# Performance work log

Hardware: AMD Instinct MI355X
Metric: run time of the kernel (lower is better)

The kernel has to match this reference:

```python
import jax, jax.numpy as jnp
import numpy as np

EMBED_DIM = 1024
NUM_HEADS = 16
HEAD_DIM = EMBED_DIM // NUM_HEADS
B, NQ, K = 2, 2048, 2048


def setup_inputs() -> dict:
    key = jax.random.key(0)
    ks = jax.random.split(key, 11)
    s = 1.0 / np.sqrt(EMBED_DIM)
    return {
        "Q_input": jax.random.normal(ks[0], (B, NQ, EMBED_DIM), jnp.float32),
        "K_input": jax.random.normal(ks[1], (B, K, EMBED_DIM), jnp.float32),
        "V_input": jax.random.normal(ks[2], (B, K, EMBED_DIM), jnp.float32),
        "Wq": jax.random.normal(ks[3], (EMBED_DIM, EMBED_DIM), jnp.float32) * s,
        "bq": jnp.zeros((EMBED_DIM,), jnp.float32),
        "Wk": jax.random.normal(ks[4], (EMBED_DIM, EMBED_DIM), jnp.float32) * s,
        "bk": jnp.zeros((EMBED_DIM,), jnp.float32),
        "Wv": jax.random.normal(ks[5], (EMBED_DIM, EMBED_DIM), jnp.float32) * s,
        "bv": jnp.zeros((EMBED_DIM,), jnp.float32),
        "Wo": jax.random.normal(ks[6], (EMBED_DIM, EMBED_DIM), jnp.float32) * s,
        "bo": jnp.zeros((EMBED_DIM,), jnp.float32),
    }


def reference(Q_input, K_input, V_input, Wq, bq, Wk, bk, Wv, bv, Wo, bo):
    b, n_q, _ = Q_input.shape
    k = K_input.shape[1]
    # Linear projections (torch Linear: x @ W.T + b)
    Q = Q_input @ Wq.T + bq
    Kp = K_input @ Wk.T + bk
    V = V_input @ Wv.T + bv
    # [b, h, s, d]
    Q = Q.reshape(b, n_q, NUM_HEADS, HEAD_DIM).transpose(0, 2, 1, 3)
    Kp = Kp.reshape(b, k, NUM_HEADS, HEAD_DIM).transpose(0, 2, 1, 3)
    V = V.reshape(b, k, NUM_HEADS, HEAD_DIM).transpose(0, 2, 1, 3)
    scores = jnp.einsum("bhqd,bhkd->bhqk", Q, Kp) / jnp.sqrt(jnp.float32(HEAD_DIM))
    weights = jax.nn.softmax(scores, axis=-1)
    attn = jnp.einsum("bhqk,bhkd->bhqd", weights, V)
    attn = attn.transpose(0, 2, 1, 3).reshape(b, n_q, EMBED_DIM)
    return attn @ Wo.T + bo
```

## Files before the change

kernel.cpp:

```cpp
#include <hip/hip_runtime.h>
#include <hip/hip_bf16.h>

typedef __bf16  bf16x8 __attribute__((ext_vector_type(8)));
typedef float   f32x4  __attribute__((ext_vector_type(4)));
typedef float   f32x16 __attribute__((ext_vector_type(16)));

#define EMB   1024
#define QSTR  3072
#define HD    64
#define NH    16
#define SEQ   2048
#define BATCH 2
#define TOKENS (BATCH*SEQ)
#define TK    64

typedef __attribute__((address_space(1))) unsigned int* gp_t;
typedef __attribute__((address_space(3))) unsigned int* lp_t;
__device__ __forceinline__ void gload16(const __bf16* g, __bf16* l) {
    __builtin_amdgcn_global_load_lds((gp_t)(unsigned long long)(const void*)g,
                                     (lp_t)(unsigned int)(unsigned long long)(void*)l,
                                     16, 0, 0);
}

__device__ __forceinline__ unsigned int pack2(float a, float b) {
    unsigned short u0 = __builtin_bit_cast(unsigned short, (__bf16)a);
    unsigned short u1 = __builtin_bit_cast(unsigned short, (__bf16)b);
    return (unsigned int)u0 | ((unsigned int)u1 << 16);
}

__global__ __launch_bounds__(256) void cvt4_kernel(
    const float* __restrict__ s0, const float* __restrict__ s1,
    const float* __restrict__ s2, const float* __restrict__ s3,
    __bf16* __restrict__ dst, int n_per)
{
    const float* s = (blockIdx.y == 0) ? s0 : (blockIdx.y == 1) ? s1
                   : (blockIdx.y == 2) ? s2 : s3;
    int i = (blockIdx.x * 256 + threadIdx.x) * 8;
    if (i >= n_per) return;
    float4 a = *(const float4*)(s + i);
    float4 b = *(const float4*)(s + i + 4);
    __bf16 o[8] = {(__bf16)a.x, (__bf16)a.y, (__bf16)a.z, (__bf16)a.w,
                   (__bf16)b.x, (__bf16)b.y, (__bf16)b.z, (__bf16)b.w};
    *(uint4*)(dst + (size_t)blockIdx.y * n_per + i) = *(const uint4*)o;
}

__global__ __launch_bounds__(256, 3) void gemm_qkv(
    const __bf16* __restrict__ X, const __bf16* __restrict__ Wt,
    const float* __restrict__ b0, const float* __restrict__ b1,
    const float* __restrict__ b2, __bf16* __restrict__ Y)
{
    __shared__ __align__(16) __bf16 As[2][128 * 32];
    __shared__ __align__(16) __bf16 Bs[2][128 * 32];

    const int tid  = threadIdx.x;
    const int wave = tid >> 6;
    const int lane = tid & 63;
    const int quad = lane >> 4;
    const int l16  = lane & 15;
    const int warp_m = wave >> 1;
    const int warp_n = wave & 1;

    const int bm = blockIdx.y;
    const int bn = blockIdx.x;

    const int lr = lane >> 2;
    const int lc = (lane & 3) ^ ((lr >> 1) & 3);
    const __bf16* Ag = X + (size_t)(bn >> 3) * TOKENS * EMB
                         + (size_t)(bm * 128 + wave * 32 + lr) * EMB + lc * 8;
    const __bf16* Bg = Wt + (size_t)(bn * 128 + wave * 32 + lr) * EMB + lc * 8;
    const int off = wave * 1024;

    f32x4 acc[4][4] = {};

    gload16(Ag,            As[0] + off);
    gload16(Ag + 16 * EMB, As[0] + off + 512);
    gload16(Bg,            Bs[0] + off);
    gload16(Bg + 16 * EMB, Bs[0] + off + 512);

    for (int t = 0; t < EMB / 32; ++t) {
        const int cur = t & 1, nxt = cur ^ 1;
        __syncthreads();
        if (t + 1 < EMB / 32) {
            const __bf16* a0 = Ag + (t + 1) * 32;
            const __bf16* w0 = Bg + (t + 1) * 32;
            gload16(a0,            As[nxt] + off);
            gload16(a0 + 16 * EMB, As[nxt] + off + 512);
            gload16(w0,            Bs[nxt] + off);
            gload16(w0 + 16 * EMB, Bs[nxt] + off + 512);
        }

        bf16x8 af[4], bf[4];
        #pragma unroll
        for (int i = 0; i < 4; ++i) {
            int rowa = warp_m * 64 + i * 16 + l16;
            int rowb = warp_n * 64 + i * 16 + l16;
            af[i] = *(const bf16x8*)(As[cur] + (rowa * 4 + (quad ^ ((rowa >> 1) & 3))) * 8);
            bf[i] = *(const bf16x8*)(Bs[cur] + (rowb * 4 + (quad ^ ((rowb >> 1) & 3))) * 8);
        }
        #pragma unroll
        for (int i = 0; i < 4; ++i)
            #pragma unroll
            for (int j = 0; j < 4; ++j)
                acc[i][j] = __builtin_amdgcn_mfma_f32_16x16x32_bf16(af[i], bf[j], acc[i][j], 0, 0, 0);
    }

    #pragma unroll
    for (int i = 0; i < 4; ++i)
        #pragma unroll
        for (int j = 0; j < 4; ++j) {
            int n = bn * 128 + warp_n * 64 + j * 16 + l16;
            const float* bsel = (n < 1024) ? b0 : (n < 2048) ? b1 : b2;
            float bj = bsel[n & 1023];
            #pragma unroll
            for (int r = 0; r < 4; ++r) {
                int m = bm * 128 + warp_m * 64 + i * 16 + quad * 4 + r;
                Y[(size_t)m * QSTR + n] = (__bf16)(acc[i][j][r] + bj);
            }
        }
}

template <typename TY>
__global__ __launch_bounds__(256) void gemm_fast(
    const __bf16* __restrict__ X, const __bf16* __restrict__ Wt,
    const float* __restrict__ b0, TY* __restrict__ Y, int ldy)
{
    __shared__ __align__(16) __bf16 As[2][128 * 64];
    __shared__ __align__(16) __bf16 Bs[2][64 * 64];

    const int tid  = threadIdx.x;
    const int wave = tid >> 6;
    const int lane = tid & 63;
    const int quad = lane >> 4;
    const int l16  = lane & 15;
    const int warp_m = wave >> 1;
    const int warp_n = wave & 1;

    const int bm = blockIdx.y;
    const int bn = blockIdx.x;

    const int lr = lane >> 3;
    const int lc = (lane & 7) ^ lr;
    const __bf16* Ag = X + (size_t)(bm * 128 + wave * 32 + lr) * EMB + lc * 8;
    const __bf16* Bg = Wt + (size_t)(bn * 64 + wave * 16 + lr) * EMB + lc * 8;
    const int aoff = wave * 2048;
    const int boff = wave * 1024;

    f32x4 acc[4][2] = {};

    gload16(Ag,            As[0] + aoff);
    gload16(Ag +  8 * EMB, As[0] + aoff + 512);
    gload16(Ag + 16 * EMB, As[0] + aoff + 1024);
    gload16(Ag + 24 * EMB, As[0] + aoff + 1536);
    gload16(Bg,            Bs[0] + boff);
    gload16(Bg +  8 * EMB, Bs[0] + boff + 512);

    for (int t = 0; t < EMB / 64; ++t) {
        const int cur = t & 1, nxt = cur ^ 1;
        __syncthreads();
        if (t + 1 < EMB / 64) {
            const __bf16* a0 = Ag + (t + 1) * 64;
            const __bf16* w0 = Bg + (t + 1) * 64;
            gload16(a0,            As[nxt] + aoff);
            gload16(a0 +  8 * EMB, As[nxt] + aoff + 512);
            gload16(a0 + 16 * EMB, As[nxt] + aoff + 1024);
            gload16(a0 + 24 * EMB, As[nxt] + aoff + 1536);
            gload16(w0,            Bs[nxt] + boff);
            gload16(w0 +  8 * EMB, Bs[nxt] + boff + 512);
        }

        #pragma unroll
        for (int kk = 0; kk < 2; ++kk) {
            bf16x8 af[4], bf[2];
            #pragma unroll
            for (int i = 0; i < 4; ++i) {
                int row = warp_m * 64 + i * 16 + l16;
                af[i] = *(const bf16x8*)(As[cur] + (row * 8 + ((kk * 4 + quad) ^ (row & 7))) * 8);
            }
            #pragma unroll
            for (int j = 0; j < 2; ++j) {
                int row = warp_n * 32 + j * 16 + l16;
                bf[j] = *(const bf16x8*)(Bs[cur] + (row * 8 + ((kk * 4 + quad) ^ (row & 7))) * 8);
            }
            #pragma unroll
            for (int i = 0; i < 4; ++i)
                #pragma unroll
                for (int j = 0; j < 2; ++j)
                    acc[i][j] = __builtin_amdgcn_mfma_f32_16x16x32_bf16(af[i], bf[j], acc[i][j], 0, 0, 0);
        }
    }

    #pragma unroll
    for (int i = 0; i < 4; ++i)
        #pragma unroll
        for (int j = 0; j < 2; ++j) {
            int n = bn * 64 + warp_n * 32 + j * 16 + l16;
            float bj = b0[n];
            #pragma unroll
            for (int r = 0; r < 4; ++r) {
                int m = bm * 128 + warp_m * 64 + i * 16 + quad * 4 + r;
                Y[(size_t)m * ldy + n] = (TY)(acc[i][j][r] + bj);
            }
        }
}

__global__ __launch_bounds__(256) void attn_kernel(
    const __bf16* __restrict__ QKV, __bf16* __restrict__ Op)
{
    __shared__ __align__(16) __bf16 Ks[2][64][64];
    __shared__ __align__(16) __bf16 Vt[2][64][72];

    const int tid  = threadIdx.x;
    const int wave = tid >> 6;
    const int lane = tid & 63;
    const int l31  = lane & 31;
    const int hi   = lane >> 5;
    const int e7   = l31 & 7;

    const int qt = blockIdx.x;
    const int h  = blockIdx.y;
    const int b  = blockIdx.z;

    const size_t qoff  = (size_t)b * SEQ * QSTR + (size_t)h * HD;
    const size_t obase = (size_t)b * SEQ * EMB  + (size_t)h * HD;
    const int qbase = qt * 128 + wave * 32;

    bf16x8 aq[4];
    {
        const __bf16* qrow = QKV + qoff + (size_t)(qbase + l31) * QSTR + hi * 8;
        #pragma unroll
        for (int dc = 0; dc < 4; ++dc) {
            bf16x8 v = *(const bf16x8*)(qrow + dc * 16);
            #pragma unroll
            for (int i = 0; i < 8; ++i) v[i] = (__bf16)((float)v[i] * 0.125f);
            aq[dc] = v;
        }
    }

    float  l_run   = 0.f;
    f32x16 oacc[2] = {};

    const __bf16* Kg = QKV + qoff + EMB;
    const __bf16* Vg = QKV + qoff + 2 * EMB;

    const int srow = tid >> 3;
    const int scol = (tid & 7) << 3;
    const int sch  = tid & 7;
    const int kp0  = (sch ^ (srow & 7)) << 3;
    const int g0 = srow >> 3;
    const int g1 = g0 + 4;

    {
        uint4 k0 = *(const uint4*)(Kg + (size_t)(srow     ) * QSTR + scol);
        uint4 k1 = *(const uint4*)(Kg + (size_t)(srow + 32) * QSTR + scol);
        uint4 v0 = *(const uint4*)(Vg + (size_t)(srow     ) * QSTR + scol);
        uint4 v1 = *(const uint4*)(Vg + (size_t)(srow + 32) * QSTR + scol);
        *(uint4*)&Ks[0][srow     ][kp0] = k0;
        *(uint4*)&Ks[0][srow + 32][kp0] = k1;
        const __bf16* p0 = (const __bf16*)&v0;
        const __bf16* p1 = (const __bf16*)&v1;
        #pragma unroll
        for (int j = 0; j < 8; ++j) {
            int d  = scol + j;
            int gg = (d >> 3) & 7;
            Vt[0][d][((g0 ^ gg) << 3) + (srow & 7)] = p0[j];
            Vt[0][d][((g1 ^ gg) << 3) + (srow & 7)] = p1[j];
        }
    }
    __syncthreads();

    for (int t = 0; t < SEQ / TK; ++t) {
        const int cur = t & 1, nxt = cur ^ 1;
        const bool have_next = (t + 1) < SEQ / TK;
        uint4 nk0, nk1, nv0, nv1;
        if (have_next) {
            int kb = (t + 1) * TK;
            nk0 = *(const uint4*)(Kg + (size_t)(kb + srow     ) * QSTR + scol);
            nk1 = *(const uint4*)(Kg + (size_t)(kb + srow + 32) * QSTR + scol);
            nv0 = *(const uint4*)(Vg + (size_t)(kb + srow     ) * QSTR + scol);
            nv1 = *(const uint4*)(Vg + (size_t)(kb + srow + 32) * QSTR + scol);
        }

        f32x16 s[2] = {};
        __builtin_amdgcn_s_setprio(1);
        #pragma unroll
        for (int kt = 0; kt < 2; ++kt)
            #pragma unroll
            for (int dc = 0; dc < 4; ++dc) {
                bf16x8 kf = *(const bf16x8*)&Ks[cur][kt * 32 + l31][((2 * dc + hi) ^ e7) << 3];
                s[kt] = __builtin_amdgcn_mfma_f32_32x32x16_bf16(kf, aq[dc], s[kt], 0, 0, 0);
            }
        __builtin_amdgcn_s_setprio(0);

        unsigned int pw[2][4][2];
        #pragma unroll
        for (int kt = 0; kt < 2; ++kt)
            #pragma unroll
            for (int bq = 0; bq < 4; ++bq) {
                float e0 = __expf(s[kt][bq * 4 + 0]);
                float e1 = __expf(s[kt][bq * 4 + 1]);
                float e2 = __expf(s[kt][bq * 4 + 2]);
                float e3 = __expf(s[kt][bq * 4 + 3]);
                l_run += (e0 + e1) + (e2 + e3);
                pw[kt][bq][0] = pack2(e0, e1);
                pw[kt][bq][1] = pack2(e2, e3);
            }

        bf16x8 paf[4];
        #pragma unroll
        for (int kt = 0; kt < 2; ++kt)
            #pragma unroll
            for (int m = 0; m < 2; ++m) {
                unsigned x0 = pw[kt][2 * m][0],     x1 = pw[kt][2 * m][1];
                unsigned y0 = pw[kt][2 * m + 1][0], y1 = pw[kt][2 * m + 1][1];
                unsigned px0 = __shfl_xor(x0, 32, 64), px1 = __shfl_xor(x1, 32, 64);
                unsigned py0 = __shfl_xor(y0, 32, 64), py1 = __shfl_xor(y1, 32, 64);
                uint4 fw;
                fw.x = hi ? py0 : x0;
                fw.y = hi ? py1 : x1;
                fw.z = hi ? y0  : px0;
                fw.w = hi ? y1  : px1;
                paf[kt * 2 + m] = __builtin_bit_cast(bf16x8, fw);
            }

        __builtin_amdgcn_s_setprio(1);
        #pragma unroll
        for (int dh = 0; dh < 2; ++dh) {
            const int d  = dh * 32 + l31;
            const int gg = (d >> 3) & 7;
            #pragma unroll
            for (int ks = 0; ks < 4; ++ks) {
                bf16x8 bvf = *(const bf16x8*)&Vt[cur][d][((2 * ks + hi) ^ gg) << 3];
                oacc[dh] = __builtin_amdgcn_mfma_f32_32x32x16_bf16(paf[ks], bvf, oacc[dh], 0, 0, 0);
            }
        }
        __builtin_amdgcn_s_setprio(0);

        if (have_next) {
            *(uint4*)&Ks[nxt][srow     ][kp0] = nk0;
            *(uint4*)&Ks[nxt][srow + 32][kp0] = nk1;
            const __bf16* p0 = (const __bf16*)&nv0;
            const __bf16* p1 = (const __bf16*)&nv1;
            #pragma unroll
            for (int j = 0; j < 8; ++j) {
                int d  = scol + j;
                int gg = (d >> 3) & 7;
                Vt[nxt][d][((g0 ^ gg) << 3) + (srow & 7)] = p0[j];
                Vt[nxt][d][((g1 ^ gg) << 3) + (srow & 7)] = p1[j];
            }
        }
        __syncthreads();
    }

    float lf = l_run + __shfl_xor(l_run, 32, 64);

    #pragma unroll
    for (int r = 0; r < 16; ++r) {
        int qr = (r & 3) + 8 * (r >> 2) + 4 * hi;
        float lq = __shfl(lf, qr, 64);
        #pragma unroll
        for (int dh = 0; dh < 2; ++dh)
            Op[obase + (size_t)(qbase + qr) * EMB + dh * 32 + l31] =
                (__bf16)(oacc[dh][r] / lq);
    }
}

extern "C" void kernel_launch(void* const* d_in, const int* in_sizes, int n_in,
                              void* d_out, int out_size, void* d_ws, size_t ws_size,
                              hipStream_t stream) {
    const float* Qin = (const float*)d_in[0];
    const float* Kin = (const float*)d_in[1];
    const float* Vin = (const float*)d_in[2];
    const float* Wq  = (const float*)d_in[3];
    const float* bq  = (const float*)d_in[4];
    const float* Wk  = (const float*)d_in[5];
    const float* bk  = (const float*)d_in[6];
    const float* Wv  = (const float*)d_in[7];
    const float* bv  = (const float*)d_in[8];
    const float* Wo  = (const float*)d_in[9];
    const float* bo  = (const float*)d_in[10];

    const size_t TENS = (size_t)TOKENS * EMB;
    const size_t WEL  = (size_t)EMB * EMB;
    __bf16* ws = (__bf16*)d_ws;
    __bf16* Xin  = ws;
    __bf16* Wb   = ws + 3 * TENS;
    __bf16* QKVp = ws + 3 * TENS + 4 * WEL;
    __bf16* Ap   = ws;

    cvt4_kernel<<<dim3((unsigned)(TENS / 2048), 3), 256, 0, stream>>>(
        Qin, Kin, Vin, Vin, Xin, (int)TENS);
    cvt4_kernel<<<dim3((unsigned)(WEL / 2048), 4), 256, 0, stream>>>(
        Wq, Wk, Wv, Wo, Wb, (int)WEL);

    gemm_qkv<<<dim3(QSTR / 128, TOKENS / 128), 256, 0, stream>>>(
        Xin, Wb, bq, bk, bv, QKVp);

    attn_kernel<<<dim3(SEQ / 128, NH, BATCH), 256, 0, stream>>>(QKVp, Ap);

    gemm_fast<float><<<dim3(EMB / 64, TOKENS / 128), 256, 0, stream>>>(
        Ap, Wb + 3 * WEL, bo, (float*)d_out, EMB);
}
```

Measured before the change: 234.5 us.

## Pre-transpose V in global memory and stream K/V via direct-to-LDS loads

Adds a separate kernel that transposes the V projection into a per-head [d][seq] layout in the workspace. The attention kernel then fills its double-buffered K and V tiles with asynchronous global-to-LDS loads instead of register staging and scalar transposed LDS writes. This removes the per-element V transpose and register pressure from the attention inner loop. The cost is an extra kernel launch plus an extra round trip of V through global memory. There is also a risk that the single barrier per iteration does not ensure the async loads have landed before the tile is read.

```diff
diff --git a/kernel.cpp b/kernel.cpp
--- a/kernel.cpp
+++ b/kernel.cpp
@@ -203,11 +203,40 @@
         }
 }
 
+__global__ __launch_bounds__(256) void transpose_v(
+    const __bf16* __restrict__ QKV, __bf16* __restrict__ VtG)
+{
+    __shared__ __bf16 T[64][144];
+    const int tid = threadIdx.x;
+    const int tt  = blockIdx.x;
+    const int h   = blockIdx.y;
+    const int b   = blockIdx.z;
+    const __bf16* src = QKV + (size_t)b * SEQ * QSTR + (size_t)tt * 128 * QSTR
+                      + 2 * EMB + h * HD;
+    const int r = tid >> 3;
+    const int c = (tid & 7) << 3;
+    #pragma unroll
+    for (int it = 0; it < 4; ++it) {
+        uint4 v = *(const uint4*)(src + (size_t)(it * 32 + r) * QSTR + c);
+        const __bf16* p = (const __bf16*)&v;
+        #pragma unroll
+        for (int j = 0; j < 8; ++j) T[c + j][it * 32 + r] = p[j];
+    }
+    __syncthreads();
+    const int d  = tid >> 2;
+    const int t0 = (tid & 3) << 5;
+    __bf16* dst = VtG + ((size_t)(b * NH + h) * HD + d) * SEQ + tt * 128 + t0;
+    #pragma unroll
+    for (int j = 0; j < 4; ++j)
+        *(uint4*)(dst + j * 8) = *(const uint4*)&T[d][t0 + j * 8];
+}
+
 __global__ __launch_bounds__(256) void attn_kernel(
-    const __bf16* __restrict__ QKV, __bf16* __restrict__ Op)
+    const __bf16* __restrict__ QKV, const __bf16* __restrict__ VtG,
+    __bf16* __restrict__ Op)
 {
-    __shared__ __align__(16) __bf16 Ks[2][64][64];
-    __shared__ __align__(16) __bf16 Vt[2][64][72];
+    __shared__ __align__(16) __bf16 Ks[2][64 * 64];
+    __shared__ __align__(16) __bf16 Vs[2][64 * 64];
 
     const int tid  = threadIdx.x;
     const int wave = tid >> 6;
@@ -239,45 +268,27 @@
     float  l_run   = 0.f;
     f32x16 oacc[2] = {};
 
-    const __bf16* Kg = QKV + qoff + EMB;
-    const __bf16* Vg = QKV + qoff + 2 * EMB;
-
-    const int srow = tid >> 3;
-    const int scol = (tid & 7) << 3;
-    const int sch  = tid & 7;
-    const int kp0  = (sch ^ (srow & 7)) << 3;
-    const int g0 = srow >> 3;
-    const int g1 = g0 + 4;
-
-    {
-        uint4 k0 = *(const uint4*)(Kg + (size_t)(srow     ) * QSTR + scol);
-        uint4 k1 = *(const uint4*)(Kg + (size_t)(srow + 32) * QSTR + scol);
-        uint4 v0 = *(const uint4*)(Vg + (size_t)(srow     ) * QSTR + scol);
-        uint4 v1 = *(const uint4*)(Vg + (size_t)(srow + 32) * QSTR + scol);
-        *(uint4*)&Ks[0][srow     ][kp0] = k0;
-        *(uint4*)&Ks[0][srow + 32][kp0] = k1;
-        const __bf16* p0 = (const __bf16*)&v0;
-        const __bf16* p1 = (const __bf16*)&v1;
-        #pragma unroll
-        for (int j = 0; j < 8; ++j) {
-            int d  = scol + j;
-            int gg = (d >> 3) & 7;
-            Vt[0][d][((g0 ^ gg) << 3) + (srow & 7)] = p0[j];
-            Vt[0][d][((g1 ^ gg) << 3) + (srow & 7)] = p1[j];
-        }
-    }
-    __syncthreads();
+    const int r8 = tid >> 3, c8 = tid & 7;
+    const int cl = ((c8 ^ (r8 & 7)) << 3);
+    const __bf16* Kg0 = QKV + qoff + EMB + (size_t)r8 * QSTR + cl;
+    const __bf16* Vg0 = VtG + (size_t)(b * NH + h) * HD * SEQ
+                            + (size_t)r8 * SEQ + cl;
+    const int ldsoff = wave * 512;
+
+    gload16(Kg0,                 Ks[0] + ldsoff);
+    gload16(Kg0 + 32 * QSTR,     Ks[0] + 2048 + ldsoff);
+    gload16(Vg0,                 Vs[0] + ldsoff);
+    gload16(Vg0 + 32 * SEQ,      Vs[0] + 2048 + ldsoff);
 
     for (int t = 0; t < SEQ / TK; ++t) {
         const int cur = t & 1, nxt = cur ^ 1;
-        const bool have_next = (t + 1) < SEQ / TK;
-        uint4 nk0, nk1, nv0, nv1;
-        if (have_next) {
-            int kb = (t + 1) * TK;
-            nk0 = *(const uint4*)(Kg + (size_t)(kb + srow     ) * QSTR + scol);
-            nk1 = *(const uint4*)(Kg + (size_t)(kb + srow + 32) * QSTR + scol);
-            nv0 = *(const uint4*)(Vg + (size_t)(kb + srow     ) * QSTR + scol);
-            nv1 = *(const uint4*)(Vg + (size_t)(kb + srow + 32) * QSTR + scol);
+        __syncthreads();
+        if (t + 1 < SEQ / TK) {
+            const int kb = (t + 1) * TK;
+            gload16(Kg0 + (size_t)kb * QSTR,              Ks[nxt] + ldsoff);
+            gload16(Kg0 + (size_t)(kb + 32) * QSTR,       Ks[nxt] + 2048 + ldsoff);
+            gload16(Vg0 + kb,                             Vs[nxt] + ldsoff);
+            gload16(Vg0 + 32 * SEQ + kb,                  Vs[nxt] + 2048 + ldsoff);
         }
 
         f32x16 s[2] = {};
@@ -286,7 +297,8 @@
         for (int kt = 0; kt < 2; ++kt)
             #pragma unroll
             for (int dc = 0; dc < 4; ++dc) {
-                bf16x8 kf = *(const bf16x8*)&Ks[cur][kt * 32 + l31][((2 * dc + hi) ^ e7) << 3];
+                bf16x8 kf = *(const bf16x8*)(Ks[cur] + (kt * 32 + l31) * 64
+                                             + (((2 * dc + hi) ^ e7) << 3));
                 s[kt] = __builtin_amdgcn_mfma_f32_32x32x16_bf16(kf, aq[dc], s[kt], 0, 0, 0);
             }
         __builtin_amdgcn_s_setprio(0);
@@ -324,31 +336,14 @@
 
         __builtin_amdgcn_s_setprio(1);
         #pragma unroll
-        for (int dh = 0; dh < 2; ++dh) {
-            const int d  = dh * 32 + l31;
-            const int gg = (d >> 3) & 7;
+        for (int dh = 0; dh < 2; ++dh)
             #pragma unroll
             for (int ks = 0; ks < 4; ++ks) {
-                bf16x8 bvf = *(const bf16x8*)&Vt[cur][d][((2 * ks + hi) ^ gg) << 3];
+                bf16x8 bvf = *(const bf16x8*)(Vs[cur] + (dh * 32 + l31) * 64
+                                              + (((2 * ks + hi) ^ e7) << 3));
                 oacc[dh] = __builtin_amdgcn_mfma_f32_32x32x16_bf16(paf[ks], bvf, oacc[dh], 0, 0, 0);
             }
-        }
         __builtin_amdgcn_s_setprio(0);
-
-        if (have_next) {
-            *(uint4*)&Ks[nxt][srow     ][kp0] = nk0;
-            *(uint4*)&Ks[nxt][srow + 32][kp0] = nk1;
-            const __bf16* p0 = (const __bf16*)&nv0;
-            const __bf16* p1 = (const __bf16*)&nv1;
-            #pragma unroll
-            for (int j = 0; j < 8; ++j) {
-                int d  = scol + j;
-                int gg = (d >> 3) & 7;
-                Vt[nxt][d][((g0 ^ gg) << 3) + (srow & 7)] = p0[j];
-                Vt[nxt][d][((g1 ^ gg) << 3) + (srow & 7)] = p1[j];
-            }
-        }
-        __syncthreads();
     }
 
     float lf = l_run + __shfl_xor(l_run, 32, 64);
@@ -386,6 +381,7 @@
     __bf16* Wb   = ws + 3 * TENS;
     __bf16* QKVp = ws + 3 * TENS + 4 * WEL;
     __bf16* Ap   = ws;
+    __bf16* VtG  = ws + TENS;
 
     cvt4_kernel<<<dim3((unsigned)(TENS / 2048), 3), 256, 0, stream>>>(
         Qin, Kin, Vin, Vin, Xin, (int)TENS);
@@ -395,7 +391,9 @@
     gemm_qkv<<<dim3(QSTR / 128, TOKENS / 128), 256, 0, stream>>>(
         Xin, Wb, bq, bk, bv, QKVp);
 
-    attn_kernel<<<dim3(SEQ / 128, NH, BATCH), 256, 0, stream>>>(QKVp, Ap);
+    transpose_v<<<dim3(SEQ / 128, NH, BATCH), 256, 0, stream>>>(QKVp, VtG);
+
+    attn_kernel<<<dim3(SEQ / 128, NH, BATCH), 256, 0, stream>>>(QKVp, VtG, Ap);
 
     gemm_fast<float><<<dim3(EMB / 64, TOKENS / 128), 256, 0, stream>>>(
         Ap, Wb + 3 * WEL, bo, (float*)d_out, EMB);
```

Result: no change. 237.7 us (+1.4%).

## Emit V pre-transposed from QKV GEMM and stream K/V via async LDS loads

Applied to the files above, without the earlier changes.

The QKV projection epilogue now writes the V third transposed per head (d-major, token-contiguous) through an LDS staging tile into the V columns of the QKV buffer. The attention kernel can then load K and V tiles straight into LDS with global_load_lds instead of register loads plus a scalar transpose scatter. The K tile also grows to 128 keys, processed as two halves per iteration, which halves the number of barriers. The costs are a more complex GEMM epilogue with extra syncs and a reinterpreted QKV buffer layout that the rest of the pipeline must match.

```diff
diff --git a/kernel.cpp b/kernel.cpp
--- a/kernel.cpp
+++ b/kernel.cpp
@@ -12,7 +12,7 @@
 #define SEQ   2048
 #define BATCH 2
 #define TOKENS (BATCH*SEQ)
-#define TK    64
+#define TK    128
 
 typedef __attribute__((address_space(1))) unsigned int* gp_t;
 typedef __attribute__((address_space(3))) unsigned int* lp_t;
@@ -49,8 +49,7 @@
     const float* __restrict__ b0, const float* __restrict__ b1,
     const float* __restrict__ b2, __bf16* __restrict__ Y)
 {
-    __shared__ __align__(16) __bf16 As[2][128 * 32];
-    __shared__ __align__(16) __bf16 Bs[2][128 * 32];
+    __shared__ __align__(16) __bf16 SMEM[4 * 128 * 32];
 
     const int tid  = threadIdx.x;
     const int wave = tid >> 6;
@@ -72,10 +71,10 @@
 
     f32x4 acc[4][4] = {};
 
-    gload16(Ag,            As[0] + off);
-    gload16(Ag + 16 * EMB, As[0] + off + 512);
-    gload16(Bg,            Bs[0] + off);
-    gload16(Bg + 16 * EMB, Bs[0] + off + 512);
+    gload16(Ag,            SMEM + off);
+    gload16(Ag + 16 * EMB, SMEM + off + 512);
+    gload16(Bg,            SMEM + 8192 + off);
+    gload16(Bg + 16 * EMB, SMEM + 8192 + off + 512);
 
     for (int t = 0; t < EMB / 32; ++t) {
         const int cur = t & 1, nxt = cur ^ 1;
@@ -83,19 +82,21 @@
         if (t + 1 < EMB / 32) {
             const __bf16* a0 = Ag + (t + 1) * 32;
             const __bf16* w0 = Bg + (t + 1) * 32;
-            gload16(a0,            As[nxt] + off);
-            gload16(a0 + 16 * EMB, As[nxt] + off + 512);
-            gload16(w0,            Bs[nxt] + off);
-            gload16(w0 + 16 * EMB, Bs[nxt] + off + 512);
-        }
-
+            gload16(a0,            SMEM + nxt * 4096 + off);
+            gload16(a0 + 16 * EMB, SMEM + nxt * 4096 + off + 512);
+            gload16(w0,            SMEM + 8192 + nxt * 4096 + off);
+            gload16(w0 + 16 * EMB, SMEM + 8192 + nxt * 4096 + off + 512);
+        }
+
+        const __bf16* Acur = SMEM + cur * 4096;
+        const __bf16* Bcur = SMEM + 8192 + cur * 4096;
         bf16x8 af[4], bf[4];
         #pragma unroll
         for (int i = 0; i < 4; ++i) {
             int rowa = warp_m * 64 + i * 16 + l16;
             int rowb = warp_n * 64 + i * 16 + l16;
-            af[i] = *(const bf16x8*)(As[cur] + (rowa * 4 + (quad ^ ((rowa >> 1) & 3))) * 8);
-            bf[i] = *(const bf16x8*)(Bs[cur] + (rowb * 4 + (quad ^ ((rowb >> 1) & 3))) * 8);
+            af[i] = *(const bf16x8*)(Acur + (rowa * 4 + (quad ^ ((rowa >> 1) & 3))) * 8);
+            bf[i] = *(const bf16x8*)(Bcur + (rowb * 4 + (quad ^ ((rowb >> 1) & 3))) * 8);
         }
         #pragma unroll
         for (int i = 0; i < 4; ++i)
@@ -104,19 +105,57 @@
                 acc[i][j] = __builtin_amdgcn_mfma_f32_16x16x32_bf16(af[i], bf[j], acc[i][j], 0, 0, 0);
     }
 
-    #pragma unroll
-    for (int i = 0; i < 4; ++i)
-        #pragma unroll
-        for (int j = 0; j < 4; ++j) {
-            int n = bn * 128 + warp_n * 64 + j * 16 + l16;
-            const float* bsel = (n < 1024) ? b0 : (n < 2048) ? b1 : b2;
-            float bj = bsel[n & 1023];
-            #pragma unroll
-            for (int r = 0; r < 4; ++r) {
-                int m = bm * 128 + warp_m * 64 + i * 16 + quad * 4 + r;
-                Y[(size_t)m * QSTR + n] = (__bf16)(acc[i][j][r] + bj);
-            }
-        }
+    if (bn < 16) {
+        #pragma unroll
+        for (int i = 0; i < 4; ++i)
+            #pragma unroll
+            for (int j = 0; j < 4; ++j) {
+                int n = bn * 128 + warp_n * 64 + j * 16 + l16;
+                const float* bsel = (n < 1024) ? b0 : b1;
+                float bj = bsel[n & 1023];
+                #pragma unroll
+                for (int r = 0; r < 4; ++r) {
+                    int m = bm * 128 + warp_m * 64 + i * 16 + quad * 4 + r;
+                    Y[(size_t)m * QSTR + n] = (__bf16)(acc[i][j][r] + bj);
+                }
+            }
+    } else {
+        __bf16* T = SMEM;
+        const int b_   = bm >> 4;
+        const int tokl = (bm & 15) * 128;
+        #pragma unroll
+        for (int half = 0; half < 2; ++half) {
+            __syncthreads();
+            if (warp_m == half) {
+                #pragma unroll
+                for (int i = 0; i < 4; ++i)
+                    #pragma unroll
+                    for (int j = 0; j < 4; ++j) {
+                        int nl = warp_n * 64 + j * 16 + l16;
+                        float bj = b2[(bn & 7) * 128 + nl];
+                        #pragma unroll
+                        for (int r = 0; r < 4; ++r) {
+                            int ml = i * 16 + quad * 4 + r;
+                            T[nl * 72 + ml] = (__bf16)(acc[i][j][r] + bj);
+                        }
+                    }
+            }
+            __syncthreads();
+            {
+                const int nl  = tid >> 1;
+                const int seg = tid & 1;
+                const int hh  = (bn - 16) * 2 + (nl >> 6);
+                const int dd  = nl & 63;
+                const int tok0 = tokl + half * 64 + seg * 32;
+                const int bh_ = b_ * NH + hh;
+                __bf16* dst = Y + ((size_t)((bh_ * 64 + dd) * 2 + (tok0 >> 10))) * QSTR
+                                + 2048 + (tok0 & 1023);
+                #pragma unroll
+                for (int k = 0; k < 4; ++k)
+                    *(uint4*)(dst + k * 8) = *(const uint4*)&T[nl * 72 + seg * 32 + k * 8];
+            }
+        }
+    }
 }
 
 template <typename TY>
@@ -206,8 +245,8 @@
 __global__ __launch_bounds__(256) void attn_kernel(
     const __bf16* __restrict__ QKV, __bf16* __restrict__ Op)
 {
-    __shared__ __align__(16) __bf16 Ks[2][64][64];
-    __shared__ __align__(16) __bf16 Vt[2][64][72];
+    __shared__ __align__(16) __bf16 Ks[2][128 * 64];
+    __shared__ __align__(16) __bf16 Vs[2][64 * 128];
 
     const int tid  = threadIdx.x;
     const int wave = tid >> 6;
@@ -223,6 +262,7 @@
     const size_t qoff  = (size_t)b * SEQ * QSTR + (size_t)h * HD;
     const size_t obase = (size_t)b * SEQ * EMB  + (size_t)h * HD;
     const int qbase = qt * 128 + wave * 32;
+    const int bh = b * NH + h;
 
     bf16x8 aq[4];
     {
@@ -239,116 +279,93 @@
     float  l_run   = 0.f;
     f32x16 oacc[2] = {};
 
-    const __bf16* Kg = QKV + qoff + EMB;
-    const __bf16* Vg = QKV + qoff + 2 * EMB;
-
-    const int srow = tid >> 3;
-    const int scol = (tid & 7) << 3;
-    const int sch  = tid & 7;
-    const int kp0  = (sch ^ (srow & 7)) << 3;
-    const int g0 = srow >> 3;
-    const int g1 = g0 + 4;
-
-    {
-        uint4 k0 = *(const uint4*)(Kg + (size_t)(srow     ) * QSTR + scol);
-        uint4 k1 = *(const uint4*)(Kg + (size_t)(srow + 32) * QSTR + scol);
-        uint4 v0 = *(const uint4*)(Vg + (size_t)(srow     ) * QSTR + scol);
-        uint4 v1 = *(const uint4*)(Vg + (size_t)(srow + 32) * QSTR + scol);
-        *(uint4*)&Ks[0][srow     ][kp0] = k0;
-        *(uint4*)&Ks[0][srow + 32][kp0] = k1;
-        const __bf16* p0 = (const __bf16*)&v0;
-        const __bf16* p1 = (const __bf16*)&v1;
-        #pragma unroll
-        for (int j = 0; j < 8; ++j) {
-            int d  = scol + j;
-            int gg = (d >> 3) & 7;
-            Vt[0][d][((g0 ^ gg) << 3) + (srow & 7)] = p0[j];
-            Vt[0][d][((g1 ^ gg) << 3) + (srow & 7)] = p1[j];
-        }
-    }
-    __syncthreads();
+    const int kr = tid >> 3;
+    const int kc = ((tid & 7) ^ (kr & 7)) << 3;
+    const __bf16* Kg0 = QKV + qoff + EMB + (size_t)kr * QSTR + kc;
+    const int vr  = tid >> 4;
+    const int vpc = tid & 15;
+    const int vlc = (vpc & 8) | ((vpc ^ vr) & 7);
+    const __bf16* Vg0 = QKV + ((size_t)(bh * 64 + vr) * 2) * QSTR + 2048 + vlc * 8;
+
+    #define STAGE(buf, kb)                                                        \
+        {                                                                         \
+            _Pragma("unroll")                                                     \
+            for (int i_ = 0; i_ < 4; ++i_)                                        \
+                gload16(Kg0 + (size_t)((kb) + i_ * 32) * QSTR,                    \
+                        Ks[buf] + i_ * 2048 + tid * 8);                           \
+            const size_t vt_ = (size_t)((kb) >> 10) * QSTR + ((kb) & 1023);       \
+            _Pragma("unroll")                                                     \
+            for (int i_ = 0; i_ < 4; ++i_)                                        \
+                gload16(Vg0 + (size_t)i_ * 32 * QSTR + vt_,                       \
+                        Vs[buf] + i_ * 2048 + tid * 8);                           \
+        }
+
+    STAGE(0, 0);
 
     for (int t = 0; t < SEQ / TK; ++t) {
         const int cur = t & 1, nxt = cur ^ 1;
-        const bool have_next = (t + 1) < SEQ / TK;
-        uint4 nk0, nk1, nv0, nv1;
-        if (have_next) {
-            int kb = (t + 1) * TK;
-            nk0 = *(const uint4*)(Kg + (size_t)(kb + srow     ) * QSTR + scol);
-            nk1 = *(const uint4*)(Kg + (size_t)(kb + srow + 32) * QSTR + scol);
-            nv0 = *(const uint4*)(Vg + (size_t)(kb + srow     ) * QSTR + scol);
-            nv1 = *(const uint4*)(Vg + (size_t)(kb + srow + 32) * QSTR + scol);
-        }
-
-        f32x16 s[2] = {};
-        __builtin_amdgcn_s_setprio(1);
-        #pragma unroll
-        for (int kt = 0; kt < 2; ++kt)
-            #pragma unroll
-            for (int dc = 0; dc < 4; ++dc) {
-                bf16x8 kf = *(const bf16x8*)&Ks[cur][kt * 32 + l31][((2 * dc + hi) ^ e7) << 3];
-                s[kt] = __builtin_amdgcn_mfma_f32_32x32x16_bf16(kf, aq[dc], s[kt], 0, 0, 0);
-            }
-        __builtin_amdgcn_s_setprio(0);
-
-        unsigned int pw[2][4][2];
-        #pragma unroll
-        for (int kt = 0; kt < 2; ++kt)
-            #pragma unroll
-            for (int bq = 0; bq < 4; ++bq) {
-                float e0 = __expf(s[kt][bq * 4 + 0]);
-                float e1 = __expf(s[kt][bq * 4 + 1]);
-                float e2 = __expf(s[kt][bq * 4 + 2]);
-                float e3 = __expf(s[kt][bq * 4 + 3]);
-                l_run += (e0 + e1) + (e2 + e3);
-                pw[kt][bq][0] = pack2(e0, e1);
-                pw[kt][bq][1] = pack2(e2, e3);
-            }
-
-        bf16x8 paf[4];
-        #pragma unroll
-        for (int kt = 0; kt < 2; ++kt)
-            #pragma unroll
-            for (int m = 0; m < 2; ++m) {
-                unsigned x0 = pw[kt][2 * m][0],     x1 = pw[kt][2 * m][1];
-                unsigned y0 = pw[kt][2 * m + 1][0], y1 = pw[kt][2 * m + 1][1];
-                unsigned px0 = __shfl_xor(x0, 32, 64), px1 = __shfl_xor(x1, 32, 64);
-                unsigned py0 = __shfl_xor(y0, 32, 64), py1 = __shfl_xor(y1, 32, 64);
-                uint4 fw;
-                fw.x = hi ? py0 : x0;
-                fw.y = hi ? py1 : x1;
-                fw.z = hi ? y0  : px0;
-                fw.w = hi ? y1  : px1;
-                paf[kt * 2 + m] = __builtin_bit_cast(bf16x8, fw);
-            }
-
-        __builtin_amdgcn_s_setprio(1);
-        #pragma unroll
-        for (int dh = 0; dh < 2; ++dh) {
-            const int d  = dh * 32 + l31;
-            const int gg = (d >> 3) & 7;
-            #pragma unroll
-            for (int ks = 0; ks < 4; ++ks) {
-                bf16x8 bvf = *(const bf16x8*)&Vt[cur][d][((2 * ks + hi) ^ gg) << 3];
-                oacc[dh] = __builtin_amdgcn_mfma_f32_32x32x16_bf16(paf[ks], bvf, oacc[dh], 0, 0, 0);
-            }
-        }
-        __builtin_amdgcn_s_setprio(0);
-
-        if (have_next) {
-            *(uint4*)&Ks[nxt][srow     ][kp0] = nk0;
-            *(uint4*)&Ks[nxt][srow + 32][kp0] = nk1;
-            const __bf16* p0 = (const __bf16*)&nv0;
-            const __bf16* p1 = (const __bf16*)&nv1;
-            #pragma unroll
-            for (int j = 0; j < 8; ++j) {
-                int d  = scol + j;
-                int gg = (d >> 3) & 7;
-                Vt[nxt][d][((g0 ^ gg) << 3) + (srow & 7)] = p0[j];
-                Vt[nxt][d][((g1 ^ gg) << 3) + (srow & 7)] = p1[j];
-            }
-        }
         __syncthreads();
+        if (t + 1 < SEQ / TK) STAGE(nxt, (t + 1) * TK);
+
+        #pragma unroll
+        for (int half = 0; half < 2; ++half) {
+            const __bf16* Kh = Ks[cur] + half * 4096;
+            const int vco = half * 8;
+
+            f32x16 s[2] = {};
+            __builtin_amdgcn_s_setprio(1);
+            #pragma unroll
+            for (int kt = 0; kt < 2; ++kt)
+                #pragma unroll
+                for (int dc = 0; dc < 4; ++dc) {
+                    bf16x8 kf = *(const bf16x8*)(Kh + (kt * 32 + l31) * 64
+                                                 + (((2 * dc + hi) ^ e7) << 3));
+                    s[kt] = __builtin_amdgcn_mfma_f32_32x32x16_bf16(kf, aq[dc], s[kt], 0, 0, 0);
+                }
+            __builtin_amdgcn_s_setprio(0);
+
+            unsigned int pw[2][4][2];
+            #pragma unroll
+            for (int kt = 0; kt < 2; ++kt)
+                #pragma unroll
+                for (int bq = 0; bq < 4; ++bq) {
+                    float e0 = __expf(s[kt][bq * 4 + 0]);
+                    float e1 = __expf(s[kt][bq * 4 + 1]);
+                    float e2 = __expf(s[kt][bq * 4 + 2]);
+                    float e3 = __expf(s[kt][bq * 4 + 3]);
+                    l_run += (e0 + e1) + (e2 + e3);
+                    pw[kt][bq][0] = pack2(e0, e1);
+                    pw[kt][bq][1] = pack2(e2, e3);
+                }
+
+            bf16x8 paf[4];
+            #pragma unroll
+            for (int kt = 0; kt < 2; ++kt)
+                #pragma unroll
+                for (int m = 0; m < 2; ++m) {
+                    unsigned x0 = pw[kt][2 * m][0],     x1 = pw[kt][2 * m][1];
+                    unsigned y0 = pw[kt][2 * m + 1][0], y1 = pw[kt][2 * m + 1][1];
+                    unsigned px0 = __shfl_xor(x0, 32, 64), px1 = __shfl_xor(x1, 32, 64);
+                    unsigned py0 = __shfl_xor(y0, 32, 64), py1 = __shfl_xor(y1, 32, 64);
+                    uint4 fw;
+                    fw.x = hi ? py0 : x0;
+                    fw.y = hi ? py1 : x1;
+                    fw.z = hi ? y0  : px0;
+                    fw.w = hi ? y1  : px1;
+                    paf[kt * 2 + m] = __builtin_bit_cast(bf16x8, fw);
+                }
+
+            __builtin_amdgcn_s_setprio(1);
+            #pragma unroll
+            for (int dh = 0; dh < 2; ++dh)
+                #pragma unroll
+                for (int ks = 0; ks < 4; ++ks) {
+                    bf16x8 bvf = *(const bf16x8*)(Vs[cur] + (dh * 32 + l31) * 128
+                                                  + ((vco + ((2 * ks + hi) ^ e7)) << 3));
+                    oacc[dh] = __builtin_amdgcn_mfma_f32_32x32x16_bf16(paf[ks], bvf, oacc[dh], 0, 0, 0);
+                }
+            __builtin_amdgcn_s_setprio(0);
+        }
     }
 
     float lf = l_run + __shfl_xor(l_run, 32, 64);
@@ -362,6 +379,7 @@
             Op[obase + (size_t)(qbase + qr) * EMB + dh * 32 + l31] =
                 (__bf16)(oacc[dh][r] / lq);
     }
+    #undef STAGE
 }
 
 extern "C" void kernel_launch(void* const* d_in, const int* in_sizes, int n_in,
```

Result: faster. 229.5 us (-2.2%).
